# Kernel optimization log

Measured on AMD Instinct MI355X. Metric: run time of the kernel, lower is better.

## Reference

```python
import jax, jax.numpy as jnp
import numpy as np

FEATURE_DIM = 1024
N_CONCEPTS = 32768
BATCH = 1024
TEMPERATURE = 0.1
EPS = 1e-12  # matches torch F.normalize eps


def l2_normalize(x, axis=-1):
    n = jnp.linalg.norm(x, axis=axis, keepdims=True)
    return x / jnp.maximum(n, EPS)


def setup_inputs() -> dict:
    key = jax.random.key(0)
    k1, k2, k3, k4 = jax.random.split(key, 4)
    features = jax.random.normal(k1, (BATCH, FEATURE_DIM), dtype=jnp.float32)
    # Linear projection params (original inits to identity/zeros; random exercises the math)
    W = jnp.eye(FEATURE_DIM, dtype=jnp.float32) + 0.02 * jax.random.normal(k2, (FEATURE_DIM, FEATURE_DIM), dtype=jnp.float32)
    b = 0.01 * jax.random.normal(k3, (FEATURE_DIM,), dtype=jnp.float32)
    prototypes = l2_normalize(jax.random.normal(k4, (N_CONCEPTS, FEATURE_DIM), dtype=jnp.float32))
    return {"features": features, "W": W, "b": b, "prototypes": prototypes}


def reference(features, W, b, prototypes):
    # projection: features @ W.T + b   (torch nn.Linear convention)
    projected = jnp.einsum('bd,ed->be', features, W) + b          # [B, D]
    projected = l2_normalize(projected)                           # [B, D]
    # cosine similarity against all prototypes
    similarities = jnp.einsum('bd,kd->bk', projected, prototypes) # [B, K]
    activations = jax.nn.softmax(similarities / TEMPERATURE, axis=-1)
    best_idx = jnp.argmax(similarities, axis=-1)                  # [B] int
    return activations, best_idx
```

## Files before the change

### kernel.cpp

```cpp
#include <hip/hip_runtime.h>
#include <hip/hip_bf16.h>


typedef __attribute__((ext_vector_type(8))) short short8;
typedef __attribute__((ext_vector_type(4))) float floatx4;

__device__ __forceinline__ unsigned short f2bf(float f) {
  unsigned int u = __float_as_uint(f);
  u += 0x7fffu + ((u >> 16) & 1u);
  return (unsigned short)(u >> 16);
}
__device__ __forceinline__ float bf2f(unsigned short h) {
  return __uint_as_float(((unsigned int)h) << 16);
}

__global__ __launch_bounds__(256) void cvt_f32_bf16(
    const float* __restrict__ src, unsigned short* __restrict__ dst, int n8) {
  int i = blockIdx.x * blockDim.x + threadIdx.x;
  if (i >= n8) return;
  const float4* s4 = (const float4*)src;
  float4 a = s4[2 * i];
  float4 b = s4[2 * i + 1];
  short8 o;
  o[0] = (short)f2bf(a.x); o[1] = (short)f2bf(a.y);
  o[2] = (short)f2bf(a.z); o[3] = (short)f2bf(a.w);
  o[4] = (short)f2bf(b.x); o[5] = (short)f2bf(b.y);
  o[6] = (short)f2bf(b.z); o[7] = (short)f2bf(b.w);
  ((short8*)dst)[i] = o;
}

__global__ __launch_bounds__(256) void cvt_split3(
    const float* __restrict__ src, unsigned short* __restrict__ H,
    unsigned short* __restrict__ Md, unsigned short* __restrict__ L, int n4) {
  int i = blockIdx.x * blockDim.x + threadIdx.x;
  if (i >= n4) return;
  float4 x = ((const float4*)src)[i];
  ushort4 h, m, l;
  float v, r;
  v = x.x; h.x = f2bf(v); r = v - bf2f(h.x); m.x = f2bf(r); l.x = f2bf(r - bf2f(m.x));
  v = x.y; h.y = f2bf(v); r = v - bf2f(h.y); m.y = f2bf(r); l.y = f2bf(r - bf2f(m.y));
  v = x.z; h.z = f2bf(v); r = v - bf2f(h.z); m.z = f2bf(r); l.z = f2bf(r - bf2f(m.z));
  v = x.w; h.w = f2bf(v); r = v - bf2f(h.w); m.w = f2bf(r); l.w = f2bf(r - bf2f(m.w));
  ((ushort4*)H)[i] = h; ((ushort4*)Md)[i] = m; ((ushort4*)L)[i] = l;
}


#define BARRIER() asm volatile("s_barrier" ::: "memory")
#define WAITLGKM()                                        \
  do {                                                    \
    asm volatile("s_waitcnt lgkmcnt(0)" ::: "memory");    \
    __builtin_amdgcn_sched_barrier(0);                    \
  } while (0)
#define WAITVM4() asm volatile("s_waitcnt vmcnt(4)" ::: "memory")

#define STAGE(OP, SLOT, H, KT)                                                 \
  do {                                                                         \
    const unsigned short* _s0 = (OP ? pB0 : pA0) + (H)*131072 + (KT)*64;       \
    const unsigned short* _s1 = (OP ? pB1 : pA1) + (H)*131072 + (KT)*64;       \
    __builtin_amdgcn_global_load_lds(                                          \
        (const __attribute__((address_space(1))) void*)_s0,                    \
        (__attribute__((address_space(3))) void*)(&lds[SLOT][OP][(H)*8192 + w * 512]), \
        16, 0, 0);                                                             \
    __builtin_amdgcn_global_load_lds(                                          \
        (const __attribute__((address_space(1))) void*)_s1,                    \
        (__attribute__((address_space(3))) void*)(&lds[SLOT][OP][(H)*8192 + 4096 + w * 512]), \
        16, 0, 0);                                                             \
  } while (0)

#define READ4(dst, base, off, rowadd)                                          \
  _Pragma("unroll") for (int q = 0; q < 4; q++)                                \
      dst[q] = *(const short8*)((base) + (off) + ((rowadd) + q) * 2048);

#define MFMA16(AB, BB, MBASE)                                                  \
  do {                                                                         \
    __builtin_amdgcn_sched_barrier(0);                                         \
    __builtin_amdgcn_s_setprio(1);                                             \
    _Pragma("unroll") for (int mf = 0; mf < 4; mf++)                           \
        _Pragma("unroll") for (int nf = 0; nf < 4; nf++)                       \
            acc[(MBASE) + mf][nf] = __builtin_amdgcn_mfma_f32_16x16x32_bf16(   \
                AB[mf], BB[nf], acc[(MBASE) + mf][nf], 0, 0, 0);               \
    __builtin_amdgcn_s_setprio(0);                                             \
    __builtin_amdgcn_sched_barrier(0);                                         \
  } while (0)

__global__ __launch_bounds__(512, 2) void gemm_nt_bf16_256(
    const unsigned short* __restrict__ A, const unsigned short* __restrict__ B,
    float* __restrict__ C, int M, int N, int K) {
  __shared__ unsigned short lds[2][2][16384];
  const int tid = threadIdx.x;
  const int w = tid >> 6, lane = tid & 63;
  const int wr = w >> 2, wc = w & 3;
  const int fr = lane & 15, koff8 = lane >> 4;

  const int bid = blockIdx.x;
  const int c8 = bid & 7, u = bid >> 3;
  const long tn = (long)(c8 * 16 + (u >> 2)) * 256;
  const long tm = (long)(u & 3) * 256;

  const int idx0 = w * 64 + lane;
  const int idx1 = 512 + idx0;
  const int rh0 = idx0 >> 3, sc0 = (idx0 & 7) ^ (rh0 & 7);
  const int rh1 = idx1 >> 3, sc1 = (idx1 & 7) ^ (rh1 & 7);
  const unsigned short* pA0 = A + (tm + rh0) * 1024 + sc0 * 8;
  const unsigned short* pA1 = A + (tm + rh1) * 1024 + sc1 * 8;
  const unsigned short* pB0 = B + (tn + rh0) * 1024 + sc0 * 8;
  const unsigned short* pB1 = B + (tn + rh1) * 1024 + sc1 * 8;

  const int rA = wr * 128 + fr;
  const int rB = wc * 64 + fr;
  const int offA0 = rA * 128 + ((koff8 ^ (rA & 7)) << 4);
  const int offA1 = rA * 128 + (((koff8 ^ 4) ^ (rA & 7)) << 4);
  const int offB0 = rB * 128 + ((koff8 ^ (rB & 7)) << 4);
  const int offB1 = rB * 128 + (((koff8 ^ 4) ^ (rB & 7)) << 4);

  const char* ldsc = (const char*)&lds[0][0][0];
#define LDSA(s) (ldsc + (s)*65536)
#define LDSB(s) (ldsc + (s)*65536 + 32768)

  floatx4 acc[8][4];
#pragma unroll
  for (int i = 0; i < 8; i++)
#pragma unroll
    for (int j = 0; j < 4; j++) acc[i][j] = (floatx4){0.f, 0.f, 0.f, 0.f};

  short8 a0[4], a1[4], a2[4], b0[4], b1[4];

  STAGE(0, 0, 0, 0); STAGE(0, 0, 1, 0); STAGE(1, 0, 0, 0); STAGE(1, 0, 1, 0);
  STAGE(0, 1, 0, 1); STAGE(0, 1, 1, 1);
  WAITVM4();
  BARRIER();

#pragma unroll 1
  for (int i = 0; i < 8; i++) {
    const int t1 = 2 * i + 1;
    const int t2 = (2 * i + 2) & 15;
    const int t3 = (2 * i + 3) & 15;

    READ4(a0, LDSA(0), offA0, 0);
    READ4(a1, LDSA(0), offA0, 4);
    READ4(b0, LDSB(0), offB0, 0);
    STAGE(1, 1, 0, t1);
    BARRIER(); WAITLGKM();
    MFMA16(a0, b0, 0);
    BARRIER();
    READ4(a0, LDSA(0), offA1, 0);
    READ4(a2, LDSA(0), offA1, 4);
    READ4(b1, LDSB(0), offB1, 0);
    STAGE(1, 1, 1, t1);
    BARRIER(); WAITLGKM();
    MFMA16(a1, b0, 4);
    BARRIER();
    STAGE(0, 0, 0, t2);
    BARRIER();
    MFMA16(a0, b1, 0);
    BARRIER();
    STAGE(0, 0, 1, t2);
    WAITVM4();
    BARRIER();
    MFMA16(a2, b1, 4);
    BARRIER();

    READ4(a0, LDSA(1), offA0, 0);
    READ4(a1, LDSA(1), offA0, 4);
    READ4(b0, LDSB(1), offB0, 0);
    STAGE(1, 0, 0, t2);
    BARRIER(); WAITLGKM();
    MFMA16(a0, b0, 0);
    BARRIER();
    READ4(a0, LDSA(1), offA1, 0);
    READ4(a2, LDSA(1), offA1, 4);
    READ4(b1, LDSB(1), offB1, 0);
    STAGE(1, 0, 1, t2);
    BARRIER(); WAITLGKM();
    MFMA16(a1, b0, 4);
    BARRIER();
    STAGE(0, 1, 0, t3);
    BARRIER();
    MFMA16(a0, b1, 0);
    BARRIER();
    STAGE(0, 1, 1, t3);
    WAITVM4();
    BARRIER();
    MFMA16(a2, b1, 4);
    BARRIER();
  }

  const long crow = tm + wr * 128 + ((lane >> 4) * 4);
  const long ccol = tn + wc * 64 + fr;
#pragma unroll
  for (int mf = 0; mf < 8; mf++)
#pragma unroll
    for (int nf = 0; nf < 4; nf++)
#pragma unroll
      for (int r = 0; r < 4; r++)
        C[(crow + mf * 16 + r) * (long)N + ccol + nf * 16] = acc[mf][nf][r];
#undef LDSA
#undef LDSB
}

__global__ __launch_bounds__(256) void gemm_split6_nt(
    const unsigned short* __restrict__ Ah, const unsigned short* __restrict__ Am,
    const unsigned short* __restrict__ Al, const unsigned short* __restrict__ Bh,
    const unsigned short* __restrict__ Bm, const unsigned short* __restrict__ Bl,
    float* __restrict__ Cpart, int M, int N, int K) {
  __shared__ unsigned short sA[3][64 * 32];
  __shared__ unsigned short sB[3][64 * 32];
  const int tid  = threadIdx.x;
  const int wave = tid >> 6;
  const int lane = tid & 63;
  const long tm = (long)blockIdx.y * 64;
  const long tn = (long)blockIdx.x * 64;
  const int wm = (wave & 1) * 32;
  const int wn = (wave >> 1) * 32;
  const int ksize = K / gridDim.z;
  const int kbase = blockIdx.z * ksize;
  float* C = Cpart + (size_t)blockIdx.z * M * N;

  floatx4 accH[2][2], accL[2][2];
#pragma unroll
  for (int i = 0; i < 2; i++)
#pragma unroll
    for (int j = 0; j < 2; j++) {
      accH[i][j] = (floatx4){0.f, 0.f, 0.f, 0.f};
      accL[i][j] = (floatx4){0.f, 0.f, 0.f, 0.f};
    }

  const int rstage = tid >> 2;
  const int cstage = (tid & 3) * 8;
  const long aoff = (tm + rstage) * (long)K + cstage;
  const long boff = (tn + rstage) * (long)K + cstage;
  const unsigned short* Asrc[3] = {Ah + aoff, Am + aoff, Al + aoff};
  const unsigned short* Bsrc[3] = {Bh + boff, Bm + boff, Bl + boff};

  for (int k0 = kbase; k0 < kbase + ksize; k0 += 32) {
#pragma unroll
    for (int p = 0; p < 3; p++) {
      __builtin_amdgcn_global_load_lds(
          (const __attribute__((address_space(1))) void*)(Asrc[p] + k0),
          (__attribute__((address_space(3))) void*)(sA[p] + wave * 512), 16, 0, 0);
      __builtin_amdgcn_global_load_lds(
          (const __attribute__((address_space(1))) void*)(Bsrc[p] + k0),
          (__attribute__((address_space(3))) void*)(sB[p] + wave * 512), 16, 0, 0);
    }
    __syncthreads();

    const int fr = lane & 15;
    const int koff = (lane >> 4) * 8;
    short8 a_[3][2], b_[3][2];
#pragma unroll
    for (int p = 0; p < 3; p++)
#pragma unroll
      for (int mf = 0; mf < 2; mf++) {
        a_[p][mf] = *(const short8*)(sA[p] + (wm + mf * 16 + fr) * 32 + koff);
        b_[p][mf] = *(const short8*)(sB[p] + (wn + mf * 16 + fr) * 32 + koff);
      }
#pragma unroll
    for (int mf = 0; mf < 2; mf++)
#pragma unroll
      for (int nf = 0; nf < 2; nf++) {
        accH[mf][nf] = __builtin_amdgcn_mfma_f32_16x16x32_bf16(
            a_[0][mf], b_[0][nf], accH[mf][nf], 0, 0, 0);
        accL[mf][nf] = __builtin_amdgcn_mfma_f32_16x16x32_bf16(
            a_[0][mf], b_[1][nf], accL[mf][nf], 0, 0, 0);
        accL[mf][nf] = __builtin_amdgcn_mfma_f32_16x16x32_bf16(
            a_[1][mf], b_[0][nf], accL[mf][nf], 0, 0, 0);
        accL[mf][nf] = __builtin_amdgcn_mfma_f32_16x16x32_bf16(
            a_[0][mf], b_[2][nf], accL[mf][nf], 0, 0, 0);
        accL[mf][nf] = __builtin_amdgcn_mfma_f32_16x16x32_bf16(
            a_[2][mf], b_[0][nf], accL[mf][nf], 0, 0, 0);
        accL[mf][nf] = __builtin_amdgcn_mfma_f32_16x16x32_bf16(
            a_[1][mf], b_[1][nf], accL[mf][nf], 0, 0, 0);
      }
    __syncthreads();
  }

  const long crow = tm + wm + ((lane >> 4) * 4);
  const long ccol = tn + wn + (lane & 15);
#pragma unroll
  for (int mf = 0; mf < 2; mf++)
#pragma unroll
    for (int nf = 0; nf < 2; nf++)
#pragma unroll
      for (int r = 0; r < 4; r++)
        C[(crow + mf * 16 + r) * (long)N + ccol + nf * 16] =
            accH[mf][nf][r] + accL[mf][nf][r];
}

__global__ __launch_bounds__(256) void norm_bias_rows(
    const float* __restrict__ P0, const float* __restrict__ P1, int nparts,
    const float* __restrict__ bias, unsigned short* __restrict__ Pn,
    float* __restrict__ Pn32) {
  const int b = blockIdx.x, tid = threadIdx.x;
  float4 v = ((const float4*)(P0 + (long)b * 1024))[tid];
  if (nparts == 2) {
    float4 v1 = ((const float4*)(P1 + (long)b * 1024))[tid];
    v.x += v1.x; v.y += v1.y; v.z += v1.z; v.w += v1.w;
  }
  float4 bb = ((const float4*)bias)[tid];
  v.x += bb.x; v.y += bb.y; v.z += bb.z; v.w += bb.w;
  float ss = v.x * v.x + v.y * v.y + v.z * v.z + v.w * v.w;
#pragma unroll
  for (int off = 32; off > 0; off >>= 1) ss += __shfl_down(ss, off);
  __shared__ float wred[4];
  if ((tid & 63) == 0) wred[tid >> 6] = ss;
  __syncthreads();
  float tot = wred[0] + wred[1] + wred[2] + wred[3];
  float inv = 1.0f / fmaxf(sqrtf(tot), 1e-12f);
  float4 p = make_float4(v.x * inv, v.y * inv, v.z * inv, v.w * inv);
  ((float4*)Pn32)[b * 256 + tid] = p;
  ushort4 o;
  o.x = f2bf(p.x); o.y = f2bf(p.y); o.z = f2bf(p.z); o.w = f2bf(p.w);
  ((ushort4*)Pn)[b * 256 + tid] = o;
}

__global__ __launch_bounds__(256) void softmax_argmax_refine(
    float* __restrict__ S, const float* __restrict__ Pn32,
    const float* __restrict__ protos, float* __restrict__ idx_out) {
  const int b = blockIdx.x, tid = threadIdx.x;
  const int wave = tid >> 6, lane = tid & 63;
  float4* row4 = (float4*)(S + (long)b * 32768);

  float m = -3.4e38f, l = 0.f;
#pragma unroll 4
  for (int it = 0; it < 32; it++) {
    float4 v = row4[tid + 256 * it];
    float zx = v.x * 10.f, zy = v.y * 10.f, zz = v.z * 10.f, zw = v.w * 10.f;
    float m4 = fmaxf(fmaxf(zx, zy), fmaxf(zz, zw));
    float nm = fmaxf(m, m4);
    l = l * __expf(m - nm) + __expf(zx - nm) + __expf(zy - nm) +
        __expf(zz - nm) + __expf(zw - nm);
    m = nm;
  }
#pragma unroll
  for (int off = 1; off < 64; off <<= 1) {
    float mo = __shfl_xor(m, off);
    float lo = __shfl_xor(l, off);
    float nm = fmaxf(m, mo);
    l = l * __expf(m - nm) + lo * __expf(mo - nm);
    m = nm;
  }
  __shared__ float sm_[4], sl_[4];
  __shared__ int cand[64];
  __shared__ int ncand;
  if (lane == 0) { sm_[wave] = m; sl_[wave] = l; }
  if (tid == 0) ncand = 0;
  __syncthreads();
  float Mz = fmaxf(fmaxf(sm_[0], sm_[1]), fmaxf(sm_[2], sm_[3]));
  float L = sl_[0] * __expf(sm_[0] - Mz) + sl_[1] * __expf(sm_[1] - Mz) +
            sl_[2] * __expf(sm_[2] - Mz) + sl_[3] * __expf(sm_[3] - Mz);
  float invL = 1.0f / L;
  float thr = Mz * 0.1f - 0.012f;

#pragma unroll 4
  for (int it = 0; it < 32; it++) {
    int i4 = tid + 256 * it;
    float4 v = row4[i4];
    if (fmaxf(fmaxf(v.x, v.y), fmaxf(v.z, v.w)) >= thr) {
      if (v.x >= thr) { int p = atomicAdd(&ncand, 1); if (p < 64) cand[p] = i4 * 4; }
      if (v.y >= thr) { int p = atomicAdd(&ncand, 1); if (p < 64) cand[p] = i4 * 4 + 1; }
      if (v.z >= thr) { int p = atomicAdd(&ncand, 1); if (p < 64) cand[p] = i4 * 4 + 2; }
      if (v.w >= thr) { int p = atomicAdd(&ncand, 1); if (p < 64) cand[p] = i4 * 4 + 3; }
    }
    float4 e;
    e.x = __expf(v.x * 10.f - Mz) * invL;
    e.y = __expf(v.y * 10.f - Mz) * invL;
    e.z = __expf(v.z * 10.f - Mz) * invL;
    e.w = __expf(v.w * 10.f - Mz) * invL;
    row4[i4] = e;
  }
  __syncthreads();
  int n = ncand < 64 ? ncand : 64;

  float4 pv = ((const float4*)(Pn32 + (long)b * 1024))[tid];
  __shared__ double dred[4];
  double best = -1e300;
  int besti = 0x7fffffff;
  for (int c = 0; c < n; c++) {
    int k = cand[c];
    float4 kv = ((const float4*)(protos + (long)k * 1024))[tid];
    double d = (double)pv.x * kv.x + (double)pv.y * kv.y +
               (double)pv.z * kv.z + (double)pv.w * kv.w;
#pragma unroll
    for (int off = 32; off > 0; off >>= 1) d += __shfl_down(d, off);
    if (lane == 0) dred[wave] = d;
    __syncthreads();
    if (tid == 0) {
      double tot = dred[0] + dred[1] + dred[2] + dred[3];
      if (tot > best || (tot == best && k < besti)) { best = tot; besti = k; }
    }
    __syncthreads();
  }
  if (tid == 0) idx_out[b] = (float)besti;
}

extern "C" void kernel_launch(void* const* d_in, const int* in_sizes, int n_in,
                              void* d_out, int out_size, void* d_ws, size_t ws_size,
                              hipStream_t stream) {
  const float* features = (const float*)d_in[0];
  const float* W        = (const float*)d_in[1];
  const float* bias     = (const float*)d_in[2];
  const float* protos   = (const float*)d_in[3];

  const size_t MB = 1024 * 1024;
  char* ws = (char*)d_ws;
  unsigned short* protoB = (unsigned short*)ws;
  unsigned short* Fh = (unsigned short*)(ws + 64 * MB);
  unsigned short* Fm = (unsigned short*)(ws + 66 * MB);
  unsigned short* Fl = (unsigned short*)(ws + 68 * MB);
  unsigned short* Wh = (unsigned short*)(ws + 70 * MB);
  unsigned short* Wm = (unsigned short*)(ws + 72 * MB);
  unsigned short* Wl = (unsigned short*)(ws + 74 * MB);
  float*          P0 = (float*)(ws + 76 * MB);
  float*          P1 = (float*)(ws + 80 * MB);
  unsigned short* Pn   = (unsigned short*)(ws + 64 * MB);
  float*          Pn32 = (float*)(ws + 66 * MB);

  const int ksplit = (ws_size >= 84 * MB) ? 2 : 1;

  float* S = (float*)d_out;
  float* idx_out = S + (size_t)1024 * 32768;

  cvt_f32_bf16<<<16384, 256, 0, stream>>>(protos, protoB, 32768 * 1024 / 8);
  cvt_split3<<<1024, 256, 0, stream>>>(features, Fh, Fm, Fl, 1024 * 1024 / 4);
  cvt_split3<<<1024, 256, 0, stream>>>(W, Wh, Wm, Wl, 1024 * 1024 / 4);
  gemm_split6_nt<<<dim3(16, 16, ksplit), 256, 0, stream>>>(
      Fh, Fm, Fl, Wh, Wm, Wl, P0, 1024, 1024, 1024);
  norm_bias_rows<<<1024, 256, 0, stream>>>(P0, P1, ksplit, bias, Pn, Pn32);
  gemm_nt_bf16_256<<<512, 512, 0, stream>>>(Pn, protoB, S, 1024, 32768, 1024);
  softmax_argmax_refine<<<1024, 256, 0, stream>>>(S, Pn32, protos, idx_out);
}
```

Baseline: 410.0 us.

## Fuse per-tile softmax max/sum into GEMM epilogue and drop one similarity pass

The GEMM epilogue now computes per-row max and exp-sum partials for each 256-column tile, reduces them across waves through LDS, and writes them to a workspace buffer. The softmax kernel then combines the 128 partials per row instead of re-reading the whole 32768-wide similarity row, which removes one full read pass over the 128MB score matrix. Separately, two MFMA groups in the main loop are merged so that one barrier pair per half-iteration is removed. The cost is extra shuffle and exp work plus an LDS reduction in the GEMM epilogue, and an ml buffer that reuses the P0 workspace region.

```diff
diff --git a/kernel.cpp b/kernel.cpp
--- a/kernel.cpp
+++ b/kernel.cpp
@@ -85,7 +85,7 @@
 
 __global__ __launch_bounds__(512, 2) void gemm_nt_bf16_256(
     const unsigned short* __restrict__ A, const unsigned short* __restrict__ B,
-    float* __restrict__ C, int M, int N, int K) {
+    float* __restrict__ C, float* __restrict__ ml, int M, int N, int K) {
   __shared__ unsigned short lds[2][2][16384];
   const int tid = threadIdx.x;
   const int w = tid >> 6, lane = tid & 63;
@@ -94,7 +94,8 @@
 
   const int bid = blockIdx.x;
   const int c8 = bid & 7, u = bid >> 3;
-  const long tn = (long)(c8 * 16 + (u >> 2)) * 256;
+  const int nb = c8 * 16 + (u >> 2);
+  const long tn = (long)nb * 256;
   const long tm = (long)(u & 3) * 256;
 
   const int idx0 = w * 64 + lane;
@@ -149,11 +150,9 @@
     STAGE(1, 1, 1, t1);
     BARRIER(); WAITLGKM();
     MFMA16(a1, b0, 4);
+    MFMA16(a0, b1, 0);
     BARRIER();
     STAGE(0, 0, 0, t2);
-    BARRIER();
-    MFMA16(a0, b1, 0);
-    BARRIER();
     STAGE(0, 0, 1, t2);
     WAITVM4();
     BARRIER();
@@ -173,16 +172,48 @@
     STAGE(1, 0, 1, t2);
     BARRIER(); WAITLGKM();
     MFMA16(a1, b0, 4);
+    MFMA16(a0, b1, 0);
     BARRIER();
     STAGE(0, 1, 0, t3);
-    BARRIER();
-    MFMA16(a0, b1, 0);
-    BARRIER();
     STAGE(0, 1, 1, t3);
     WAITVM4();
     BARRIER();
     MFMA16(a2, b1, 4);
     BARRIER();
+  }
+
+  {
+    float2* mlx = (float2*)&lds[0][0][0];
+    const int hi = lane >> 4;
+#pragma unroll
+    for (int mf = 0; mf < 8; mf++)
+#pragma unroll
+      for (int r = 0; r < 4; r++) {
+        float z0 = acc[mf][0][r] * 10.f, z1 = acc[mf][1][r] * 10.f;
+        float z2 = acc[mf][2][r] * 10.f, z3 = acc[mf][3][r] * 10.f;
+        float mz = fmaxf(fmaxf(z0, z1), fmaxf(z2, z3));
+#pragma unroll
+        for (int off = 1; off < 16; off <<= 1) mz = fmaxf(mz, __shfl_xor(mz, off));
+        float ls = __expf(z0 - mz) + __expf(z1 - mz) +
+                   __expf(z2 - mz) + __expf(z3 - mz);
+#pragma unroll
+        for (int off = 1; off < 16; off <<= 1) ls += __shfl_xor(ls, off);
+        if (fr == 0) mlx[(wr * 128 + mf * 16 + hi * 4 + r) * 4 + wc] =
+            make_float2(mz, ls);
+      }
+    __syncthreads();
+    if (tid < 256) {
+      const int wrr = tid >> 7, row = tid & 127;
+      float2 q0 = mlx[(wrr * 128 + row) * 4 + 0];
+      float2 q1 = mlx[(wrr * 128 + row) * 4 + 1];
+      float2 q2 = mlx[(wrr * 128 + row) * 4 + 2];
+      float2 q3 = mlx[(wrr * 128 + row) * 4 + 3];
+      float Mb = fmaxf(fmaxf(q0.x, q1.x), fmaxf(q2.x, q3.x));
+      float Lb = q0.y * __expf(q0.x - Mb) + q1.y * __expf(q1.x - Mb) +
+                 q2.y * __expf(q2.x - Mb) + q3.y * __expf(q3.x - Mb);
+      ((float2*)ml)[(long)nb * 1024 + (tm + wrr * 128 + row)] =
+          make_float2(Mb, Lb);
+    }
   }
 
   const long crow = tm + wr * 128 + ((lane >> 4) * 4);
@@ -315,41 +346,36 @@
 
 __global__ __launch_bounds__(256) void softmax_argmax_refine(
     float* __restrict__ S, const float* __restrict__ Pn32,
-    const float* __restrict__ protos, float* __restrict__ idx_out) {
+    const float* __restrict__ protos, const float* __restrict__ ml,
+    float* __restrict__ idx_out) {
   const int b = blockIdx.x, tid = threadIdx.x;
   const int wave = tid >> 6, lane = tid & 63;
   float4* row4 = (float4*)(S + (long)b * 32768);
 
-  float m = -3.4e38f, l = 0.f;
-#pragma unroll 4
-  for (int it = 0; it < 32; it++) {
-    float4 v = row4[tid + 256 * it];
-    float zx = v.x * 10.f, zy = v.y * 10.f, zz = v.z * 10.f, zw = v.w * 10.f;
-    float m4 = fmaxf(fmaxf(zx, zy), fmaxf(zz, zw));
-    float nm = fmaxf(m, m4);
-    l = l * __expf(m - nm) + __expf(zx - nm) + __expf(zy - nm) +
-        __expf(zz - nm) + __expf(zw - nm);
-    m = nm;
-  }
-#pragma unroll
-  for (int off = 1; off < 64; off <<= 1) {
-    float mo = __shfl_xor(m, off);
-    float lo = __shfl_xor(l, off);
-    float nm = fmaxf(m, mo);
-    l = l * __expf(m - nm) + lo * __expf(mo - nm);
-    m = nm;
-  }
-  __shared__ float sm_[4], sl_[4];
+  __shared__ float2 mlred[2];
   __shared__ int cand[64];
   __shared__ int ncand;
-  if (lane == 0) { sm_[wave] = m; sl_[wave] = l; }
   if (tid == 0) ncand = 0;
+
+  if (wave < 2) {
+    float2 p = ((const float2*)ml)[(long)tid * 1024 + b];
+    float m = p.x, l = p.y;
+#pragma unroll
+    for (int off = 1; off < 64; off <<= 1) {
+      float mo = __shfl_xor(m, off);
+      float lo = __shfl_xor(l, off);
+      float nm = fmaxf(m, mo);
+      l = l * __expf(m - nm) + lo * __expf(mo - nm);
+      m = nm;
+    }
+    if (lane == 0) mlred[wave] = make_float2(m, l);
+  }
   __syncthreads();
-  float Mz = fmaxf(fmaxf(sm_[0], sm_[1]), fmaxf(sm_[2], sm_[3]));
-  float L = sl_[0] * __expf(sm_[0] - Mz) + sl_[1] * __expf(sm_[1] - Mz) +
-            sl_[2] * __expf(sm_[2] - Mz) + sl_[3] * __expf(sm_[3] - Mz);
-  float invL = 1.0f / L;
-  float thr = Mz * 0.1f - 0.012f;
+  const float m0 = mlred[0].x, m1 = mlred[1].x;
+  const float Mz = fmaxf(m0, m1);
+  const float L = mlred[0].y * __expf(m0 - Mz) + mlred[1].y * __expf(m1 - Mz);
+  const float invL = 1.0f / L;
+  const float thr = Mz * 0.1f - 0.012f;
 
 #pragma unroll 4
   for (int it = 0; it < 32; it++) {
@@ -414,6 +440,7 @@
   float*          P1 = (float*)(ws + 80 * MB);
   unsigned short* Pn   = (unsigned short*)(ws + 64 * MB);
   float*          Pn32 = (float*)(ws + 66 * MB);
+  float*          mlb  = (float*)(ws + 76 * MB);
 
   const int ksplit = (ws_size >= 84 * MB) ? 2 : 1;
 
@@ -426,6 +453,6 @@
   gemm_split6_nt<<<dim3(16, 16, ksplit), 256, 0, stream>>>(
       Fh, Fm, Fl, Wh, Wm, Wl, P0, 1024, 1024, 1024);
   norm_bias_rows<<<1024, 256, 0, stream>>>(P0, P1, ksplit, bias, Pn, Pn32);
-  gemm_nt_bf16_256<<<512, 512, 0, stream>>>(Pn, protoB, S, 1024, 32768, 1024);
-  softmax_argmax_refine<<<1024, 256, 0, stream>>>(S, Pn32, protos, idx_out);
-}
+  gemm_nt_bf16_256<<<512, 512, 0, stream>>>(Pn, protoB, S, mlb, 1024, 32768, 1024);
+  softmax_argmax_refine<<<1024, 256, 0, stream>>>(S, Pn32, protos, mlb, idx_out);
+}
```

Result: slower. 419.3 us (+2.3%).
